# Performance work log

Hardware: AMD Instinct MI355X
Metric: run time of the kernel (lower is better)

The kernel has to match this reference:

```python
import jax, jax.numpy as jnp
import numpy as np

B, N, C1, C2, H = 4, 4096, 320, 256, 5
HD = C1 // H  # 64


def setup_inputs() -> dict:
    key = jax.random.key(0)
    ks = jax.random.split(key, 9)
    w = lambda k, shape, fan_in: jax.random.normal(k, shape, jnp.float32) * (fan_in ** -0.5)
    return {
        "x1": jax.random.normal(ks[0], (B, N, C1), jnp.float32),
        "x2": jax.random.normal(ks[1], (B, N, C2), jnp.float32),
        # nn.Linear weights, torch layout [out_features, in_features]
        "q1_w": w(ks[2], (C1, C1), C1),
        "q2_w": w(ks[3], (C1, C2), C2),
        "kv1_w": w(ks[4], (2 * C1, C2), C2),
        "kv2_w": w(ks[5], (2 * C1, C1), C1),
        "proj1_w": w(ks[6], (C1, C1), C1),
        "proj1_b": jnp.zeros((C1,), jnp.float32),
        "proj2_w": w(ks[7], (C1, C1), C1),
        "proj2_b": jnp.zeros((C1,), jnp.float32),
    }


def _branch(xq, xkv, q_w, kv_w, proj_w, proj_b):
    b, n, _ = xq.shape
    scale = HD ** -0.5
    q = (xq @ q_w.T).reshape(b, n, H, HD).transpose(0, 2, 1, 3)          # [B,H,N,HD]
    kv = (xkv @ kv_w.T).reshape(b, n, 2, H, HD).transpose(2, 0, 3, 1, 4)  # [2,B,H,N,HD]
    k, v = kv[0], kv[1]
    attn = jax.nn.softmax(jnp.einsum('bhqd,bhkd->bhqk', q * scale, k), axis=-1)
    y = jnp.einsum('bhqk,bhkd->bhqd', attn, v)                            # [B,H,N,HD]
    y = y.transpose(0, 2, 1, 3).reshape(b, n, C1)
    return y @ proj_w.T + proj_b


def reference(x1, x2, q1_w, q2_w, kv1_w, kv2_w, proj1_w, proj1_b, proj2_w, proj2_b):
    y1 = _branch(x1, x2, q1_w, kv1_w, proj1_w, proj1_b)  # x1 queries, x2 keys/values
    y2 = _branch(x2, x1, q2_w, kv2_w, proj2_w, proj2_b)  # x2 queries, x1 keys/values
    return jnp.concatenate((y1, y2), axis=-1)            # [B,N,2*C1]
```

## Files before the change

kernel.cpp:

```cpp
#include <hip/hip_runtime.h>
#include <hip/hip_bf16.h>

#define Bb 4
#define Nn 4096
#define C1 320
#define C2 256
#define Hh 5
#define HD 64
#define Mm (Bb*Nn)

using bf16 = __hip_bfloat16;
typedef __attribute__((ext_vector_type(8))) short  short8;
typedef __attribute__((ext_vector_type(4))) short  short4_;
typedef __attribute__((ext_vector_type(4))) float  f32x4;

__device__ __forceinline__ short f2s(float f) {
    bf16 h = __float2bfloat16(f);
    short s;
    __builtin_memcpy(&s, &h, 2);
    return s;
}

__device__ __forceinline__ float fexp2(float x) {
#if __has_builtin(__builtin_amdgcn_exp2f)
    return __builtin_amdgcn_exp2f(x);
#else
    return exp2f(x);
#endif
}

__device__ __forceinline__ int swz(int row, int bb) {
    return row * 64 + ((bb ^ (row & 7)) << 3);
}

struct CvtArgs {
    const float* s[8];
    bf16* d[8];
    int off[9];
};

__global__ void cvt_all(CvtArgs a) {
    int i = (blockIdx.x * blockDim.x + threadIdx.x) * 4;
    if (i >= a.off[8]) return;
    int seg = 0;
    #pragma unroll
    for (int k = 1; k < 8; ++k) seg += (i >= a.off[k]);
    int j = i - a.off[seg];
    float4 v = *(const float4*)(a.s[seg] + j);
    short4_ o = { f2s(v.x), f2s(v.y), f2s(v.z), f2s(v.w) };
    *(short4_*)(a.d[seg] + j) = o;
}

__global__ __launch_bounds__(256) void gemm_bt(
    const bf16* __restrict__ A, const bf16* __restrict__ W,
    int K, int mode, float oscale,
    bf16* __restrict__ O1, bf16* __restrict__ O2,
    const float* __restrict__ bias, float* __restrict__ Of, int ooff)
{
    __shared__ bf16 la[64 * 64];
    __shared__ bf16 lw[64 * 64];
    const int m0 = blockIdx.x * 64, n0 = blockIdx.y * 64;
    const int t = threadIdx.x;
    const int wave = t >> 6, lane = t & 63, l16 = lane & 15, quad = lane >> 4;
    const int sr = t >> 3, sb = t & 7;

    f32x4 acc[4] = {{0.f,0.f,0.f,0.f},{0.f,0.f,0.f,0.f},{0.f,0.f,0.f,0.f},{0.f,0.f,0.f,0.f}};

    const int nk = K >> 6;
    short8 ra0 = *(const short8*)(A + (size_t)(m0 + sr) * K + sb * 8);
    short8 ra1 = *(const short8*)(A + (size_t)(m0 + sr + 32) * K + sb * 8);
    short8 rw0 = *(const short8*)(W + (size_t)(n0 + sr) * K + sb * 8);
    short8 rw1 = *(const short8*)(W + (size_t)(n0 + sr + 32) * K + sb * 8);

    for (int kt = 0; kt < nk; ++kt) {
        __syncthreads();
        *(short8*)&la[swz(sr, sb)]      = ra0;
        *(short8*)&la[swz(sr + 32, sb)] = ra1;
        *(short8*)&lw[swz(sr, sb)]      = rw0;
        *(short8*)&lw[swz(sr + 32, sb)] = rw1;
        __syncthreads();
        if (kt + 1 < nk) {
            const int k0 = (kt + 1) * 64;
            ra0 = *(const short8*)(A + (size_t)(m0 + sr) * K + k0 + sb * 8);
            ra1 = *(const short8*)(A + (size_t)(m0 + sr + 32) * K + k0 + sb * 8);
            rw0 = *(const short8*)(W + (size_t)(n0 + sr) * K + k0 + sb * 8);
            rw1 = *(const short8*)(W + (size_t)(n0 + sr + 32) * K + k0 + sb * 8);
        }
        const int arow = wave * 16 + l16;
        short8 a0 = *(const short8*)&la[swz(arow, quad)];
        short8 a1 = *(const short8*)&la[swz(arow, quad + 4)];
        #pragma unroll
        for (int nt = 0; nt < 4; ++nt) {
            const int brow = nt * 16 + l16;
            short8 b0 = *(const short8*)&lw[swz(brow, quad)];
            short8 b1 = *(const short8*)&lw[swz(brow, quad + 4)];
            acc[nt] = __builtin_amdgcn_mfma_f32_16x16x32_bf16(a0, b0, acc[nt], 0, 0, 0);
            acc[nt] = __builtin_amdgcn_mfma_f32_16x16x32_bf16(a1, b1, acc[nt], 0, 0, 0);
        }
    }

    const int mrow = m0 + wave * 16 + quad * 4;
    if (mode == 2) {
        #pragma unroll
        for (int nt = 0; nt < 4; ++nt) {
            int col = n0 + nt * 16 + l16;
            float bv = bias[col];
            #pragma unroll
            for (int r = 0; r < 4; ++r)
                Of[(size_t)(mrow + r) * 640 + ooff + col] = acc[nt][r] + bv;
        }
    } else if (mode == 0 || n0 < C1) {
        #pragma unroll
        for (int nt = 0; nt < 4; ++nt) {
            int col = n0 + nt * 16 + l16;
            #pragma unroll
            for (int r = 0; r < 4; ++r)
                O1[(size_t)(mrow + r) * C1 + col] = __float2bfloat16(acc[nt][r] * oscale);
        }
    } else {
        #pragma unroll
        for (int nt = 0; nt < 4; ++nt) {
            int col = n0 + nt * 16 + l16 - C1;
            int h = col >> 6, d = col & 63;
            #pragma unroll
            for (int r = 0; r < 4; ++r) {
                int m = mrow + r;
                int b = m >> 12, n = m & (Nn - 1);
                O2[((size_t)(b * Hh + h) * 64 + d) * Nn + n] = __float2bfloat16(acc[nt][r]);
            }
        }
    }
}

__global__ __launch_bounds__(256) void flash_kernel(
    const bf16* __restrict__ Q1, const bf16* __restrict__ K1,
    const bf16* __restrict__ V1, bf16* __restrict__ Y1,
    const bf16* __restrict__ Q2, const bf16* __restrict__ K2,
    const bf16* __restrict__ V2, bf16* __restrict__ Y2)
{
    __shared__ bf16 lk[64 * 64];
    __shared__ bf16 lv[64 * 64];
    __shared__ bf16 lp[4 * 32 * 64];
    const int qt = blockIdx.x, h = blockIdx.y, z = blockIdx.z;
    const int b = z & 3, branch = z >> 2;
    const bf16* Q  = branch ? Q2 : Q1;
    const bf16* Km = branch ? K2 : K1;
    const bf16* Vt = branch ? V2 : V1;
    bf16*       Y  = branch ? Y2 : Y1;

    const int t = threadIdx.x;
    const int wave = t >> 6, lane = t & 63, l16 = lane & 15, quad = lane >> 4;
    const int sr = t >> 3, sb = t & 7;

    short8 aq[2][2];
    #pragma unroll
    for (int qf = 0; qf < 2; ++qf) {
        const bf16* qptr = Q + (size_t)(b * Nn + qt * 128 + wave * 32 + qf * 16 + l16) * C1
                             + h * HD + quad * 8;
        aq[qf][0] = *(const short8*)qptr;
        aq[qf][1] = *(const short8*)(qptr + 32);
    }

    f32x4 acc[2][4];
    #pragma unroll
    for (int qf = 0; qf < 2; ++qf)
        #pragma unroll
        for (int i = 0; i < 4; ++i) acc[qf][i] = {0.f,0.f,0.f,0.f};
    float lsum[2] = {0.f, 0.f};

    const bf16* Kbase = Km + (size_t)b * Nn * C1 + h * HD;
    const bf16* Vbase = Vt + (size_t)(b * Hh + h) * 64 * Nn;
    const int wbase = wave * (32 * 64);

    short8 rk0 = *(const short8*)(Kbase + (size_t)sr * C1 + sb * 8);
    short8 rk1 = *(const short8*)(Kbase + (size_t)(sr + 32) * C1 + sb * 8);
    short8 rv0 = *(const short8*)(Vbase + (size_t)sr * Nn + sb * 8);
    short8 rv1 = *(const short8*)(Vbase + (size_t)(sr + 32) * Nn + sb * 8);

    const int NT = Nn / 64;
    for (int kt = 0; kt < NT; ++kt) {
        __syncthreads();
        *(short8*)&lk[swz(sr, sb)]      = rk0;
        *(short8*)&lk[swz(sr + 32, sb)] = rk1;
        *(short8*)&lv[swz(sr, sb)]      = rv0;
        *(short8*)&lv[swz(sr + 32, sb)] = rv1;
        __syncthreads();
        if (kt + 1 < NT) {
            const int kn = (kt + 1) * 64;
            rk0 = *(const short8*)(Kbase + (size_t)(kn + sr) * C1 + sb * 8);
            rk1 = *(const short8*)(Kbase + (size_t)(kn + sr + 32) * C1 + sb * 8);
            rv0 = *(const short8*)(Vbase + (size_t)sr * Nn + kn + sb * 8);
            rv1 = *(const short8*)(Vbase + (size_t)(sr + 32) * Nn + kn + sb * 8);
        }

        #pragma unroll
        for (int nt = 0; nt < 4; ++nt) {
            const int krow = nt * 16 + l16;
            short8 k0 = *(const short8*)&lk[swz(krow, quad)];
            short8 k1 = *(const short8*)&lk[swz(krow, quad + 4)];
            #pragma unroll
            for (int qf = 0; qf < 2; ++qf) {
                f32x4 z4 = {0.f, 0.f, 0.f, 0.f};
                z4 = __builtin_amdgcn_mfma_f32_16x16x32_bf16(k0, aq[qf][0], z4, 0, 0, 0);
                z4 = __builtin_amdgcn_mfma_f32_16x16x32_bf16(k1, aq[qf][1], z4, 0, 0, 0);
                float p0 = fexp2(z4[0]);
                float p1 = fexp2(z4[1]);
                float p2 = fexp2(z4[2]);
                float p3 = fexp2(z4[3]);
                lsum[qf] += (p0 + p1) + (p2 + p3);
                short4_ pk = { f2s(p0), f2s(p1), f2s(p2), f2s(p3) };
                const int prow = qf * 16 + l16;
                *(short4_*)&lp[wbase + swz(prow, nt * 2 + (quad >> 1)) + (quad & 1) * 4] = pk;
            }
        }

        short8 ap[2][2];
        #pragma unroll
        for (int qf = 0; qf < 2; ++qf) {
            const int prow = qf * 16 + l16;
            ap[qf][0] = *(const short8*)&lp[wbase + swz(prow, quad)];
            ap[qf][1] = *(const short8*)&lp[wbase + swz(prow, quad + 4)];
        }
        #pragma unroll
        for (int dt = 0; dt < 4; ++dt) {
            const int vrow = dt * 16 + l16;
            short8 bv0 = *(const short8*)&lv[swz(vrow, quad)];
            short8 bv1 = *(const short8*)&lv[swz(vrow, quad + 4)];
            #pragma unroll
            for (int qf = 0; qf < 2; ++qf) {
                acc[qf][dt] = __builtin_amdgcn_mfma_f32_16x16x32_bf16(ap[qf][0], bv0, acc[qf][dt], 0, 0, 0);
                acc[qf][dt] = __builtin_amdgcn_mfma_f32_16x16x32_bf16(ap[qf][1], bv1, acc[qf][dt], 0, 0, 0);
            }
        }
    }

    #pragma unroll
    for (int qf = 0; qf < 2; ++qf) {
        float l = lsum[qf];
        l += __shfl_xor(l, 16, 64);
        l += __shfl_xor(l, 32, 64);
        #pragma unroll
        for (int reg = 0; reg < 4; ++reg) {
            float lr = __shfl(l, quad * 4 + reg, 64);
            float inv = 1.0f / lr;
            size_t rowoff = (size_t)(b * Nn + qt * 128 + wave * 32 + qf * 16 + quad * 4 + reg) * C1
                          + h * HD + l16;
            #pragma unroll
            for (int dt = 0; dt < 4; ++dt)
                Y[rowoff + dt * 16] = __float2bfloat16(acc[qf][dt][reg] * inv);
        }
    }
}

extern "C" void kernel_launch(void* const* d_in, const int* in_sizes, int n_in,
                              void* d_out, int out_size, void* d_ws, size_t ws_size,
                              hipStream_t stream)
{
    const float* x1   = (const float*)d_in[0];
    const float* x2   = (const float*)d_in[1];
    const float* q1w  = (const float*)d_in[2];
    const float* q2w  = (const float*)d_in[3];
    const float* kv1w = (const float*)d_in[4];
    const float* kv2w = (const float*)d_in[5];
    const float* p1w  = (const float*)d_in[6];
    const float* p1b  = (const float*)d_in[7];
    const float* p2w  = (const float*)d_in[8];
    const float* p2b  = (const float*)d_in[9];
    float* out = (float*)d_out;

    bf16* ws = (bf16*)d_ws;
    size_t o = 0;
    bf16* x1b  = ws + o; o += (size_t)Mm * C1;
    bf16* x2b  = ws + o; o += (size_t)Mm * C2;
    bf16* wq1  = ws + o; o += C1 * C1;
    bf16* wq2  = ws + o; o += C1 * C2;
    bf16* wkv1 = ws + o; o += 2 * C1 * C2;
    bf16* wkv2 = ws + o; o += 2 * C1 * C1;
    bf16* wp1  = ws + o; o += C1 * C1;
    bf16* wp2  = ws + o; o += C1 * C1;
    bf16* Q1   = ws + o; o += (size_t)Mm * C1;
    bf16* K1   = ws + o; o += (size_t)Mm * C1;
    bf16* V1t  = ws + o; o += (size_t)Mm * C1;
    bf16* Q2   = ws + o; o += (size_t)Mm * C1;
    bf16* K2   = ws + o; o += (size_t)Mm * C1;
    bf16* V2t  = ws + o; o += (size_t)Mm * C1;
    bf16* Y1   = ws + o; o += (size_t)Mm * C1;
    bf16* Y2   = ws + o; o += (size_t)Mm * C1;
    (void)ws_size; (void)in_sizes; (void)n_in; (void)out_size;

    CvtArgs ca;
    ca.s[0] = x1;   ca.d[0] = x1b;  int n0 = Mm * C1;
    ca.s[1] = x2;   ca.d[1] = x2b;  int n1 = Mm * C2;
    ca.s[2] = q1w;  ca.d[2] = wq1;  int n2 = C1 * C1;
    ca.s[3] = q2w;  ca.d[3] = wq2;  int n3 = C1 * C2;
    ca.s[4] = kv1w; ca.d[4] = wkv1; int n4 = 2 * C1 * C2;
    ca.s[5] = kv2w; ca.d[5] = wkv2; int n5 = 2 * C1 * C1;
    ca.s[6] = p1w;  ca.d[6] = wp1;  int n6 = C1 * C1;
    ca.s[7] = p2w;  ca.d[7] = wp2;  int n7 = C1 * C1;
    int ns[8] = {n0, n1, n2, n3, n4, n5, n6, n7};
    ca.off[0] = 0;
    for (int i = 0; i < 8; ++i) ca.off[i + 1] = ca.off[i] + ns[i];
    int total = ca.off[8];
    cvt_all<<<dim3((total / 4 + 255) / 256), 256, 0, stream>>>(ca);

    const float QS = 0.125f * 1.4426950408889634f;

    gemm_bt<<<dim3(Mm / 64, C1 / 64), 256, 0, stream>>>(x1b, wq1, C1, 0, QS, Q1, nullptr, nullptr, nullptr, 0);
    gemm_bt<<<dim3(Mm / 64, (2 * C1) / 64), 256, 0, stream>>>(x2b, wkv1, C2, 1, 1.0f, K1, V1t, nullptr, nullptr, 0);
    gemm_bt<<<dim3(Mm / 64, C1 / 64), 256, 0, stream>>>(x2b, wq2, C2, 0, QS, Q2, nullptr, nullptr, nullptr, 0);
    gemm_bt<<<dim3(Mm / 64, (2 * C1) / 64), 256, 0, stream>>>(x1b, wkv2, C1, 1, 1.0f, K2, V2t, nullptr, nullptr, 0);

    flash_kernel<<<dim3(Nn / 128, Hh, 2 * Bb), 256, 0, stream>>>(Q1, K1, V1t, Y1, Q2, K2, V2t, Y2);

    gemm_bt<<<dim3(Mm / 64, C1 / 64), 256, 0, stream>>>(Y1, wp1, C1, 2, 1.0f, nullptr, nullptr, p1b, out, 0);
    gemm_bt<<<dim3(Mm / 64, C1 / 64), 256, 0, stream>>>(Y2, wp2, C1, 2, 1.0f, nullptr, nullptr, p2b, out, C1);
}
```

Measured before the change: 387.9 us.

## Halve per-wave P staging buffer and request higher occupancy in flash kernel

The per-wave LDS buffer for the softmax probabilities is halved by staging the two 16-row query fragments one after another in the same 16x64 slot instead of together. The second fragment's scores are kept in registers while the first fragment's probabilities are written and read back. Launch bounds now ask for 5 blocks per CU to get more waves in flight. In exchange, a wave-local reuse of the LDS slot adds a write-after-read ordering dependency, and the occupancy hint may force the compiler to spill registers.

```diff
diff --git a/kernel.cpp b/kernel.cpp
--- a/kernel.cpp
+++ b/kernel.cpp
@@ -132,7 +132,7 @@
     }
 }
 
-__global__ __launch_bounds__(256) void flash_kernel(
+__global__ __launch_bounds__(256, 5) void flash_kernel(
     const bf16* __restrict__ Q1, const bf16* __restrict__ K1,
     const bf16* __restrict__ V1, bf16* __restrict__ Y1,
     const bf16* __restrict__ Q2, const bf16* __restrict__ K2,
@@ -140,7 +140,7 @@
 {
     __shared__ bf16 lk[64 * 64];
     __shared__ bf16 lv[64 * 64];
-    __shared__ bf16 lp[4 * 32 * 64];
+    __shared__ bf16 lp[4 * 16 * 64];
     const int qt = blockIdx.x, h = blockIdx.y, z = blockIdx.z;
     const int b = z & 3, branch = z >> 2;
     const bf16* Q  = branch ? Q2 : Q1;
@@ -170,7 +170,7 @@
 
     const bf16* Kbase = Km + (size_t)b * Nn * C1 + h * HD;
     const bf16* Vbase = Vt + (size_t)(b * Hh + h) * 64 * Nn;
-    const int wbase = wave * (32 * 64);
+    const int wbase = wave * (16 * 64);
 
     short8 rk0 = *(const short8*)(Kbase + (size_t)sr * C1 + sb * 8);
     short8 rk1 = *(const short8*)(Kbase + (size_t)(sr + 32) * C1 + sb * 8);
@@ -193,44 +193,52 @@
             rv1 = *(const short8*)(Vbase + (size_t)(sr + 32) * Nn + kn + sb * 8);
         }
 
+        f32x4 s1[4];
         #pragma unroll
         for (int nt = 0; nt < 4; ++nt) {
             const int krow = nt * 16 + l16;
             short8 k0 = *(const short8*)&lk[swz(krow, quad)];
             short8 k1 = *(const short8*)&lk[swz(krow, quad + 4)];
-            #pragma unroll
-            for (int qf = 0; qf < 2; ++qf) {
-                f32x4 z4 = {0.f, 0.f, 0.f, 0.f};
-                z4 = __builtin_amdgcn_mfma_f32_16x16x32_bf16(k0, aq[qf][0], z4, 0, 0, 0);
-                z4 = __builtin_amdgcn_mfma_f32_16x16x32_bf16(k1, aq[qf][1], z4, 0, 0, 0);
-                float p0 = fexp2(z4[0]);
-                float p1 = fexp2(z4[1]);
-                float p2 = fexp2(z4[2]);
-                float p3 = fexp2(z4[3]);
-                lsum[qf] += (p0 + p1) + (p2 + p3);
-                short4_ pk = { f2s(p0), f2s(p1), f2s(p2), f2s(p3) };
-                const int prow = qf * 16 + l16;
-                *(short4_*)&lp[wbase + swz(prow, nt * 2 + (quad >> 1)) + (quad & 1) * 4] = pk;
-            }
-        }
-
-        short8 ap[2][2];
-        #pragma unroll
-        for (int qf = 0; qf < 2; ++qf) {
-            const int prow = qf * 16 + l16;
-            ap[qf][0] = *(const short8*)&lp[wbase + swz(prow, quad)];
-            ap[qf][1] = *(const short8*)&lp[wbase + swz(prow, quad + 4)];
-        }
+            f32x4 z0 = {0.f, 0.f, 0.f, 0.f};
+            z0 = __builtin_amdgcn_mfma_f32_16x16x32_bf16(k0, aq[0][0], z0, 0, 0, 0);
+            z0 = __builtin_amdgcn_mfma_f32_16x16x32_bf16(k1, aq[0][1], z0, 0, 0, 0);
+            f32x4 z1 = {0.f, 0.f, 0.f, 0.f};
+            z1 = __builtin_amdgcn_mfma_f32_16x16x32_bf16(k0, aq[1][0], z1, 0, 0, 0);
+            z1 = __builtin_amdgcn_mfma_f32_16x16x32_bf16(k1, aq[1][1], z1, 0, 0, 0);
+            s1[nt] = z1;
+            float p0 = fexp2(z0[0]);
+            float p1 = fexp2(z0[1]);
+            float p2 = fexp2(z0[2]);
+            float p3 = fexp2(z0[3]);
+            lsum[0] += (p0 + p1) + (p2 + p3);
+            short4_ pk = { f2s(p0), f2s(p1), f2s(p2), f2s(p3) };
+            *(short4_*)&lp[wbase + swz(l16, nt * 2 + (quad >> 1)) + (quad & 1) * 4] = pk;
+        }
+        short8 ap00 = *(const short8*)&lp[wbase + swz(l16, quad)];
+        short8 ap01 = *(const short8*)&lp[wbase + swz(l16, quad + 4)];
+
+        #pragma unroll
+        for (int nt = 0; nt < 4; ++nt) {
+            float p0 = fexp2(s1[nt][0]);
+            float p1 = fexp2(s1[nt][1]);
+            float p2 = fexp2(s1[nt][2]);
+            float p3 = fexp2(s1[nt][3]);
+            lsum[1] += (p0 + p1) + (p2 + p3);
+            short4_ pk = { f2s(p0), f2s(p1), f2s(p2), f2s(p3) };
+            *(short4_*)&lp[wbase + swz(l16, nt * 2 + (quad >> 1)) + (quad & 1) * 4] = pk;
+        }
+        short8 ap10 = *(const short8*)&lp[wbase + swz(l16, quad)];
+        short8 ap11 = *(const short8*)&lp[wbase + swz(l16, quad + 4)];
+
         #pragma unroll
         for (int dt = 0; dt < 4; ++dt) {
             const int vrow = dt * 16 + l16;
             short8 bv0 = *(const short8*)&lv[swz(vrow, quad)];
             short8 bv1 = *(const short8*)&lv[swz(vrow, quad + 4)];
-            #pragma unroll
-            for (int qf = 0; qf < 2; ++qf) {
-                acc[qf][dt] = __builtin_amdgcn_mfma_f32_16x16x32_bf16(ap[qf][0], bv0, acc[qf][dt], 0, 0, 0);
-                acc[qf][dt] = __builtin_amdgcn_mfma_f32_16x16x32_bf16(ap[qf][1], bv1, acc[qf][dt], 0, 0, 0);
-            }
+            acc[0][dt] = __builtin_amdgcn_mfma_f32_16x16x32_bf16(ap00, bv0, acc[0][dt], 0, 0, 0);
+            acc[0][dt] = __builtin_amdgcn_mfma_f32_16x16x32_bf16(ap01, bv1, acc[0][dt], 0, 0, 0);
+            acc[1][dt] = __builtin_amdgcn_mfma_f32_16x16x32_bf16(ap10, bv0, acc[1][dt], 0, 0, 0);
+            acc[1][dt] = __builtin_amdgcn_mfma_f32_16x16x32_bf16(ap11, bv1, acc[1][dt], 0, 0, 0);
         }
     }
 
```

Measured after the change: 857.8 us. 121% more time.
